# Performance work log

Hardware: AMD Instinct MI355X
Metric: run time of the kernel (lower is better)

The kernel has to match this reference:

```python
import jax, jax.numpy as jnp
import numpy as np

N = 50000       # nodes
E = 1600000     # edges (avg degree 32)
DIN = 64
DOUT = 64
DE = 16
ATT_SLOPE = 0.2   # leaky_relu slope inside attention (GAT standard)
ACT_SLOPE = 0.01  # F.leaky_relu default between layers


def setup_inputs() -> dict:
    key = jax.random.key(0)
    ks = jax.random.split(key, 16)

    def lin(k, i, o):
        return jax.random.normal(k, (i, o), jnp.float32) / np.sqrt(i).astype(np.float32)

    def vec(k, d):
        return jax.random.normal(k, (d,), jnp.float32) / np.sqrt(d).astype(np.float32)

    return {
        "X": jax.random.normal(ks[0], (N, DIN), jnp.float32),
        "edge_index": jax.random.randint(ks[1], (2, E), 0, N),
        "edge_attr": jax.random.normal(ks[2], (E, DE), jnp.float32),
        # layer 1 params
        "W1": lin(ks[3], DIN, DOUT), "We1": lin(ks[4], DE, DOUT),
        "as1": vec(ks[5], DOUT), "ad1": vec(ks[6], DOUT), "ae1": vec(ks[7], DOUT),
        "b1": jnp.zeros((DOUT,), jnp.float32),
        # layer 2 params
        "W2": lin(ks[8], DOUT, DOUT), "We2": lin(ks[9], DE, DOUT),
        "as2": vec(ks[10], DOUT), "ad2": vec(ks[11], DOUT), "ae2": vec(ks[12], DOUT),
        "b2": jnp.zeros((DOUT,), jnp.float32),
    }


def _gat_conv(x, src, dst, edge_attr, W, We, a_s, a_d, a_e, b):
    """GATConv with edge features, softmax attention over dst neighborhoods, max aggregation."""
    n = x.shape[0]
    h = x @ W                      # [N, DOUT]
    e = edge_attr @ We             # [E, DOUT]
    # per-edge attention logits
    logits = jax.nn.leaky_relu((h @ a_s)[src] + (h @ a_d)[dst] + e @ a_e, ATT_SLOPE)  # [E]
    # numerically-stable segment softmax over destination node
    m = jax.ops.segment_max(logits, dst, num_segments=n)      # [N]
    p = jnp.exp(logits - m[dst])                               # [E]
    s = jax.ops.segment_sum(p, dst, num_segments=n)            # [N]
    att = p / jnp.maximum(s[dst], 1e-16)                       # [E]
    msg = (h[src] + e) * att[:, None]                          # [E, DOUT]
    out = jax.ops.segment_max(msg, dst, num_segments=n)        # [N, DOUT], -inf for empty
    out = jnp.where(jnp.isfinite(out), out, 0.0)
    return out + b


def reference(X, edge_index, edge_attr,
              W1, We1, as1, ad1, ae1, b1,
              W2, We2, as2, ad2, ae2, b2):
    src, dst = edge_index[0], edge_index[1]
    c1 = _gat_conv(X, src, dst, edge_attr, W1, We1, as1, ad1, ae1, b1)
    c1 = jax.nn.leaky_relu(c1, ACT_SLOPE)
    c2 = _gat_conv(c1, src, dst, edge_attr, W2, We2, as2, ad2, ae2, b2)
    c2 = jax.nn.leaky_relu(c2, ACT_SLOPE)
    return c2
```

## Files before the change

kernel.cpp:

```cpp
#include <hip/hip_runtime.h>
#include <cstdint>
#include <cstddef>

#define NN 50000
#define EE 1600000
#define D  64
#define DE 16

typedef __attribute__((ext_vector_type(2))) float vf2;

__device__ __forceinline__ float bf2f(unsigned short u) {
    return __uint_as_float(((unsigned)u) << 16);
}
__device__ __forceinline__ unsigned short f2bf(float f) {
    unsigned u = __float_as_uint(f);
    unsigned r = u + 0x7FFFu + ((u >> 16) & 1u);
    return (unsigned short)(r >> 16);
}

#define HI_ILP 4
__global__ __launch_bounds__(256) void k_hist(const int* __restrict__ dst,
                                              int* __restrict__ counts) {
    int base = blockIdx.x * (256 * HI_ILP) + threadIdx.x;
    int dd[HI_ILP]; bool v[HI_ILP];
    #pragma unroll
    for (int j = 0; j < HI_ILP; j++) {
        int e = base + j * 256;
        v[j] = (e < EE);
        dd[j] = dst[v[j] ? e : 0];
    }
    #pragma unroll
    for (int j = 0; j < HI_ILP; j++)
        if (v[j]) atomicAdd(&counts[dd[j]], 1);
}

__global__ __launch_bounds__(256) void k_scanA(const int* counts, int* bsum) {
    __shared__ int tmp[256];
    int t = threadIdx.x, i = blockIdx.x * 256 + t;
    tmp[t] = (i < NN) ? counts[i] : 0;
    __syncthreads();
    for (int off = 128; off; off >>= 1) {
        if (t < off) tmp[t] += tmp[t + off];
        __syncthreads();
    }
    if (t == 0) bsum[blockIdx.x] = tmp[0];
}

__global__ __launch_bounds__(256) void k_scanB(int* bsum, int nchunks) {
    __shared__ int tmp[256];
    int t = threadIdx.x;
    int v = (t < nchunks) ? bsum[t] : 0;
    tmp[t] = v; __syncthreads();
    for (int off = 1; off < 256; off <<= 1) {
        int x = (t >= off) ? tmp[t - off] : 0;
        __syncthreads();
        tmp[t] += x;
        __syncthreads();
    }
    if (t < nchunks) bsum[t] = tmp[t] - v;
}

__global__ __launch_bounds__(256) void k_scanC(const int* counts, const int* bsumex,
                                               int* offsets, int* cursor) {
    __shared__ int tmp[256];
    int t = threadIdx.x, i = blockIdx.x * 256 + t;
    int v = (i < NN) ? counts[i] : 0;
    tmp[t] = v; __syncthreads();
    for (int off = 1; off < 256; off <<= 1) {
        int x = (t >= off) ? tmp[t - off] : 0;
        __syncthreads();
        tmp[t] += x;
        __syncthreads();
    }
    int excl = tmp[t] - v + bsumex[blockIdx.x];
    if (i < NN) { offsets[i] = excl; cursor[i] = excl; }
}

#define SC_ILP 8
__global__ __launch_bounds__(256) void k_scatter(const int* __restrict__ src,
                                                 const int* __restrict__ dst,
                                                 const float* __restrict__ ea,
                                                 const float* __restrict__ We1,
                                                 const float* __restrict__ ae1,
                                                 const float* __restrict__ We2,
                                                 const float* __restrict__ ae2,
                                                 int* __restrict__ cursor,
                                                 int4* __restrict__ recs) {
    __shared__ float wsh[32];
    int t = threadIdx.x;
    if (t < 32) {
        const float* We = (t < 16) ? We1 : We2;
        const float* ae = (t < 16) ? ae1 : ae2;
        int k = t & 15;
        float acc = 0.f;
        #pragma unroll
        for (int c = 0; c < 64; c++) acc += We[k * 64 + c] * ae[c];
        wsh[t] = acc;
    }
    __syncthreads();
    float w1r[16], w2r[16];
    #pragma unroll
    for (int j = 0; j < 16; j++) { w1r[j] = wsh[j]; w2r[j] = wsh[16 + j]; }

    int base = blockIdx.x * (256 * SC_ILP) + t;
    int dd[SC_ILP], ss[SC_ILP], pos[SC_ILP];
    bool v[SC_ILP];
    #pragma unroll
    for (int j = 0; j < SC_ILP; j++) {
        int e = base + j * 256;
        v[j] = (e < EE);
        int ec = v[j] ? e : 0;
        dd[j] = dst[ec];
        ss[j] = src[ec];
    }
    #pragma unroll
    for (int j = 0; j < SC_ILP; j++)
        if (v[j]) pos[j] = atomicAdd(&cursor[dd[j]], 1);
    #pragma unroll
    for (int j = 0; j < SC_ILP; j++) {
        if (!v[j]) continue;
        int e = base + j * 256;
        const float4* rp = (const float4*)(ea + (size_t)e * DE);
        float4 q0 = rp[0], q1 = rp[1], q2 = rp[2], q3 = rp[3];
        float ev[16] = {q0.x, q0.y, q0.z, q0.w, q1.x, q1.y, q1.z, q1.w,
                        q2.x, q2.y, q2.z, q2.w, q3.x, q3.y, q3.z, q3.w};
        float e1 = 0.f, e2 = 0.f;
        #pragma unroll
        for (int k2 = 0; k2 < 16; k2++) {
            e1 += ev[k2] * w1r[k2];
            e2 += ev[k2] * w2r[k2];
        }
        recs[pos[j]] = make_int4(ss[j], e, __float_as_int(e1), __float_as_int(e2));
    }
}

template<int IN_BF16>
__global__ __launch_bounds__(256, 4) void k_gemm(const void* xin, const float* W,
                                                 const float* a_s, const float* a_d,
                                                 unsigned short* h, float* hs, float* hd) {
    int t = threadIdx.x, lane = t & 63;
    int wid0 = blockIdx.x * 4 + (t >> 6);
    float Wcol[64];
    #pragma unroll
    for (int k = 0; k < 64; k++) Wcol[k] = W[k * 64 + lane];
    float asl = a_s[lane], adl = a_d[lane];
    for (int n0 = wid0; n0 < NN; n0 += 4096) {
        int n = __builtin_amdgcn_readfirstlane(n0);
        float acc = 0.f;
        if (IN_BF16) {
            const uint4* xr = (const uint4*)((const unsigned short*)xin + (size_t)n * 64);
            #pragma unroll
            for (int q = 0; q < 8; q++) {
                uint4 u = xr[q];
                unsigned uu[4] = {u.x, u.y, u.z, u.w};
                #pragma unroll
                for (int j = 0; j < 4; j++) {
                    acc += bf2f((unsigned short)(uu[j] & 0xFFFFu)) * Wcol[q * 8 + 2 * j];
                    acc += bf2f((unsigned short)(uu[j] >> 16))     * Wcol[q * 8 + 2 * j + 1];
                }
            }
        } else {
            const float4* xr = (const float4*)((const float*)xin + (size_t)n * 64);
            #pragma unroll
            for (int q = 0; q < 16; q++) {
                float4 u = xr[q];
                acc += u.x * Wcol[4 * q]     + u.y * Wcol[4 * q + 1]
                     + u.z * Wcol[4 * q + 2] + u.w * Wcol[4 * q + 3];
            }
        }
        h[(size_t)n * 64 + lane] = f2bf(acc);
        float ps = acc * asl, pd = acc * adl;
        #pragma unroll
        for (int off = 32; off; off >>= 1) {
            ps += __shfl_xor(ps, off);
            pd += __shfl_xor(pd, off);
        }
        if (lane == 0) { hs[n] = ps; hd[n] = pd; }
    }
}

template<int L2>
__global__ __launch_bounds__(256, 3) void k_gat(const int4* __restrict__ recs,
                                                const int* __restrict__ offsets,
                                                const int* __restrict__ counts,
                                                const float* __restrict__ hs,
                                                const float* __restrict__ hd,
                                                const unsigned short* __restrict__ h,
                                                const float* __restrict__ ea,
                                                const float* __restrict__ We,
                                                const float* __restrict__ b,
                                                void* __restrict__ outv) {
    __shared__ float4 eal[4][4][64];
    __shared__ float2 arx[4][64];
    int t = threadIdx.x, lane = t & 63, wv = t >> 6;
    int g = lane >> 4, cl = lane & 15;

    vf2 Wp[32];
    #pragma unroll
    for (int kp = 0; kp < 8; kp++) {
        float4 wa = *(const float4*)(We + (2 * kp) * 64 + 4 * cl);
        float4 wb = *(const float4*)(We + (2 * kp + 1) * 64 + 4 * cl);
        Wp[kp].x      = wa.x; Wp[kp].y      = wb.x;
        Wp[8 + kp].x  = wa.y; Wp[8 + kp].y  = wb.y;
        Wp[16 + kp].x = wa.z; Wp[16 + kp].y = wb.z;
        Wp[24 + kp].x = wa.w; Wp[24 + kp].y = wb.w;
    }

    int d = blockIdx.x * 4 + wv;
    int start = offsets[d];
    int deg = counts[d];

    if (deg == 0) {
        if (g == 0) {
            float4 bl = *(const float4*)(b + 4 * cl);
            float o0 = (bl.x >= 0.f) ? bl.x : 0.01f * bl.x;
            float o1 = (bl.y >= 0.f) ? bl.y : 0.01f * bl.y;
            float o2 = (bl.z >= 0.f) ? bl.z : 0.01f * bl.z;
            float o3 = (bl.w >= 0.f) ? bl.w : 0.01f * bl.w;
            size_t oidx = (size_t)d * D + 4 * cl;
            if (L2) *(float4*)((float*)outv + oidx) = make_float4(o0, o1, o2, o3);
            else {
                ushort4 ov = {f2bf(o0), f2bf(o1), f2bf(o2), f2bf(o3)};
                *(ushort4*)((unsigned short*)outv + oidx) = ov;
            }
        }
        return;
    }

    float hdv = hd[d];
    bool fast = (deg <= 64);
    float m, invs;

    float ninf = -__builtin_inff();
    float a0 = ninf, a1 = ninf, a2 = ninf, a3 = ninf;

    if (fast) {
        float lg = ninf;
        if (lane < deg) {
            int4 r = recs[start + lane];
            const float4* ep = (const float4*)(ea + (size_t)r.y * DE);
            float4 q0 = ep[0], q1 = ep[1], q2 = ep[2], q3 = ep[3];
            float hsv = hs[r.x];
            eal[wv][0][lane] = q0; eal[wv][1][lane] = q1;
            eal[wv][2][lane] = q2; eal[wv][3][lane] = q3;
            arx[wv][lane].y = __int_as_float(r.x);
            float ee = __int_as_float(L2 ? r.w : r.z);
            lg = hsv + hdv + ee;
            lg = (lg >= 0.f) ? lg : 0.2f * lg;
        }

        bool vC = (g < deg);
        int jC = vC ? g : 0;
        bool vN = (4 + g < deg);
        int jN = vN ? 4 + g : 0;
        int rxC = __float_as_int(arx[wv][jC].y);
        int rxN = __float_as_int(arx[wv][jN].y);
        ushort4 hvC = *(const ushort4*)(h + (size_t)rxC * D + 4 * cl);
        ushort4 hvN = *(const ushort4*)(h + (size_t)rxN * D + 4 * cl);

        m = lg;
        #pragma unroll
        for (int off = 32; off; off >>= 1) m = fmaxf(m, __shfl_xor(m, off));
        float p = __expf(lg - m);
        float s = p;
        #pragma unroll
        for (int off = 32; off; off >>= 1) s += __shfl_xor(s, off);
        invs = 1.0f / fmaxf(s, 1e-16f);
        if (lane < deg) arx[wv][lane].x = p * invs;

        float attC = arx[wv][jC].x;
        float attN = arx[wv][jN].x;

        for (int i = 0; i < deg; i += 4) {
            int jnn = i + 8 + g;
            bool vNN = (jnn < deg);
            int jNN = vNN ? jnn : 0;
            float2 arNN = arx[wv][jNN];
            int rxNN = __float_as_int(arNN.y);
            ushort4 hvNN = *(const ushort4*)(h + (size_t)rxNN * D + 4 * cl);

            vf2 acA = {0.f, 0.f}, acB = {0.f, 0.f}, acC2 = {0.f, 0.f}, acD = {0.f, 0.f};
            #pragma unroll
            for (int kq = 0; kq < 4; kq++) {
                float4 q = eal[wv][kq][jC];
                vf2 eA; eA.x = q.x; eA.y = q.y;
                vf2 eB; eB.x = q.z; eB.y = q.w;
                acA += eA * Wp[2 * kq];       acA += eB * Wp[2 * kq + 1];
                acB += eA * Wp[8 + 2 * kq];   acB += eB * Wp[8 + 2 * kq + 1];
                acC2 += eA * Wp[16 + 2 * kq]; acC2 += eB * Wp[16 + 2 * kq + 1];
                acD += eA * Wp[24 + 2 * kq];  acD += eB * Wp[24 + 2 * kq + 1];
            }
            float e0 = acA.x + acA.y, e1 = acB.x + acB.y;
            float e2 = acC2.x + acC2.y, e3 = acD.x + acD.y;
            float o0 = (bf2f(hvC.x) + e0) * attC;
            float o1 = (bf2f(hvC.y) + e1) * attC;
            float o2 = (bf2f(hvC.z) + e2) * attC;
            float o3 = (bf2f(hvC.w) + e3) * attC;
            if (vC) {
                a0 = fmaxf(a0, o0); a1 = fmaxf(a1, o1);
                a2 = fmaxf(a2, o2); a3 = fmaxf(a3, o3);
            }
            jC = jN; vC = vN; hvC = hvN; attC = attN;
            jN = jNN; vN = vNN; hvN = hvNN; attN = arNN.x;
        }
    } else {
        float mm = ninf, s = 0.f;
        for (int i = lane; i < deg; i += 64) {
            int4 r = recs[start + i];
            float ee = __int_as_float(L2 ? r.w : r.z);
            float lg = hs[r.x] + hdv + ee;
            lg = (lg >= 0.f) ? lg : 0.2f * lg;
            float mn = fmaxf(mm, lg);
            s = ((mm == mn) ? s : s * __expf(mm - mn)) + __expf(lg - mn);
            mm = mn;
        }
        #pragma unroll
        for (int off = 32; off; off >>= 1) {
            float m2 = __shfl_xor(mm, off);
            float s2 = __shfl_xor(s, off);
            float mn = fmaxf(mm, m2);
            float sa = (mm == mn) ? s : s * __expf(mm - mn);
            float sb = (m2 == mn) ? s2 : s2 * __expf(m2 - mn);
            s = sa + sb;
            mm = mn;
        }
        m = mm;
        invs = 1.0f / fmaxf(s, 1e-16f);

        for (int i = 0; i < deg; i += 4) {
            int j = i + g;
            bool valid = (j < deg);
            int jc = valid ? j : 0;
            int4 r = recs[start + jc];
            float ee = __int_as_float(L2 ? r.w : r.z);
            float lg = hs[r.x] + hdv + ee;
            lg = (lg >= 0.f) ? lg : 0.2f * lg;
            float att = __expf(lg - m) * invs;
            const float4* ep = (const float4*)(ea + (size_t)r.y * DE);
            float4 q0 = ep[0], q1 = ep[1], q2 = ep[2], q3 = ep[3];
            ushort4 hv = *(const ushort4*)(h + (size_t)r.x * D + 4 * cl);
            float4 qs[4] = {q0, q1, q2, q3};
            vf2 acA = {0.f, 0.f}, acB = {0.f, 0.f}, acC2 = {0.f, 0.f}, acD = {0.f, 0.f};
            #pragma unroll
            for (int kq = 0; kq < 4; kq++) {
                float4 q = qs[kq];
                vf2 eA; eA.x = q.x; eA.y = q.y;
                vf2 eB; eB.x = q.z; eB.y = q.w;
                acA += eA * Wp[2 * kq];       acA += eB * Wp[2 * kq + 1];
                acB += eA * Wp[8 + 2 * kq];   acB += eB * Wp[8 + 2 * kq + 1];
                acC2 += eA * Wp[16 + 2 * kq]; acC2 += eB * Wp[16 + 2 * kq + 1];
                acD += eA * Wp[24 + 2 * kq];  acD += eB * Wp[24 + 2 * kq + 1];
            }
            float e0 = acA.x + acA.y, e1 = acB.x + acB.y;
            float e2 = acC2.x + acC2.y, e3 = acD.x + acD.y;
            float o0 = (bf2f(hv.x) + e0) * att;
            float o1 = (bf2f(hv.y) + e1) * att;
            float o2 = (bf2f(hv.z) + e2) * att;
            float o3 = (bf2f(hv.w) + e3) * att;
            if (valid) {
                a0 = fmaxf(a0, o0); a1 = fmaxf(a1, o1);
                a2 = fmaxf(a2, o2); a3 = fmaxf(a3, o3);
            }
        }
    }

    #pragma unroll
    for (int off = 16; off <= 32; off <<= 1) {
        a0 = fmaxf(a0, __shfl_xor(a0, off));
        a1 = fmaxf(a1, __shfl_xor(a1, off));
        a2 = fmaxf(a2, __shfl_xor(a2, off));
        a3 = fmaxf(a3, __shfl_xor(a3, off));
    }

    if (g == 0) {
        float4 bl = *(const float4*)(b + 4 * cl);
        float o0 = a0 + bl.x, o1 = a1 + bl.y;
        float o2 = a2 + bl.z, o3 = a3 + bl.w;
        o0 = (o0 >= 0.f) ? o0 : 0.01f * o0;
        o1 = (o1 >= 0.f) ? o1 : 0.01f * o1;
        o2 = (o2 >= 0.f) ? o2 : 0.01f * o2;
        o3 = (o3 >= 0.f) ? o3 : 0.01f * o3;
        size_t oidx = (size_t)d * D + 4 * cl;
        if (L2) {
            *(float4*)((float*)outv + oidx) = make_float4(o0, o1, o2, o3);
        } else {
            ushort4 ov = {f2bf(o0), f2bf(o1), f2bf(o2), f2bf(o3)};
            *(ushort4*)((unsigned short*)outv + oidx) = ov;
        }
    }
}

extern "C" void kernel_launch(void* const* d_in, const int* in_sizes, int n_in,
                              void* d_out, int out_size, void* d_ws, size_t ws_size,
                              hipStream_t stream) {
    const float* X   = (const float*)d_in[0];
    const int*   eix = (const int*)d_in[1];
    const float* ea  = (const float*)d_in[2];
    const float* W1  = (const float*)d_in[3];
    const float* We1 = (const float*)d_in[4];
    const float* as1 = (const float*)d_in[5];
    const float* ad1 = (const float*)d_in[6];
    const float* ae1 = (const float*)d_in[7];
    const float* b1  = (const float*)d_in[8];
    const float* W2  = (const float*)d_in[9];
    const float* We2 = (const float*)d_in[10];
    const float* as2 = (const float*)d_in[11];
    const float* ad2 = (const float*)d_in[12];
    const float* ae2 = (const float*)d_in[13];
    const float* b2  = (const float*)d_in[14];

    const int* src = eix;
    const int* dst = eix + EE;

    char* w = (char*)d_ws;
    int4* recs = (int4*)w;               w += (size_t)EE * 16;
    unsigned short* hA = (unsigned short*)w; w += (size_t)NN * D * 2;
    unsigned short* hB = (unsigned short*)w; w += (size_t)NN * D * 2;
    float* hs = (float*)w;               w += (size_t)NN * 4;
    float* hd = (float*)w;               w += (size_t)NN * 4;
    int* counts = (int*)w;               w += (size_t)NN * 4;
    int* offsets = (int*)w;              w += (size_t)NN * 4;
    int* cursor = (int*)w;               w += (size_t)NN * 4;
    int* bsum = (int*)w;                 w += 256 * 4;

    const int nchunks = (NN + 255) / 256;
    const int nhblk = (EE + 256 * HI_ILP - 1) / (256 * HI_ILP);
    const int nsblk = (EE + 256 * SC_ILP - 1) / (256 * SC_ILP);

    hipMemsetAsync(counts, 0, (size_t)NN * 4, stream);
    k_hist<<<nhblk, 256, 0, stream>>>(dst, counts);
    k_scanA<<<nchunks, 256, 0, stream>>>(counts, bsum);
    k_scanB<<<1, 256, 0, stream>>>(bsum, nchunks);
    k_scanC<<<nchunks, 256, 0, stream>>>(counts, bsum, offsets, cursor);
    k_scatter<<<nsblk, 256, 0, stream>>>(src, dst, ea, We1, ae1, We2, ae2, cursor, recs);

    k_gemm<0><<<1024, 256, 0, stream>>>(X, W1, as1, ad1, hA, hs, hd);
    k_gat<0><<<NN / 4, 256, 0, stream>>>(recs, offsets, counts, hs, hd, hA, ea, We1, b1, hB);
    k_gemm<1><<<1024, 256, 0, stream>>>(hB, W2, as2, ad2, hB, hs, hd);
    k_gat<1><<<NN / 4, 256, 0, stream>>>(recs, offsets, counts, hs, hd, hB, ea, We2, b2,
                                         (float*)d_out);
}
```

Baseline: 627.2 us.

## Fold block-sum scan into scanC and merge layer-1 GEMM with edge scatter

Removes the separate single-block scan kernel by having every scanC block redundantly scan the block sums in shared memory. Merges the layer-1 node GEMM and the edge scatter into one launch: the first 1024 blocks compute h, hs and hd, and the remaining blocks do the CSR scatter. The two independent phases can then overlap on the GPU and two launches go away. Scatter ILP drops from 8 to 2, which raises the scatter block count, and shared memory per block grows to 16KB for all blocks, including the scatter ones that do not need it.

```diff
diff --git a/kernel.cpp b/kernel.cpp
--- a/kernel.cpp
+++ b/kernel.cpp
@@ -46,24 +46,22 @@
     if (t == 0) bsum[blockIdx.x] = tmp[0];
 }
 
-__global__ __launch_bounds__(256) void k_scanB(int* bsum, int nchunks) {
+__global__ __launch_bounds__(256) void k_scanC(const int* counts, const int* bsum,
+                                               int nchunks, int* offsets, int* cursor) {
+    __shared__ int tmpb[256];
     __shared__ int tmp[256];
     int t = threadIdx.x;
-    int v = (t < nchunks) ? bsum[t] : 0;
-    tmp[t] = v; __syncthreads();
+    int bv = (t < nchunks) ? bsum[t] : 0;
+    tmpb[t] = bv; __syncthreads();
     for (int off = 1; off < 256; off <<= 1) {
-        int x = (t >= off) ? tmp[t - off] : 0;
-        __syncthreads();
-        tmp[t] += x;
-        __syncthreads();
-    }
-    if (t < nchunks) bsum[t] = tmp[t] - v;
-}
-
-__global__ __launch_bounds__(256) void k_scanC(const int* counts, const int* bsumex,
-                                               int* offsets, int* cursor) {
-    __shared__ int tmp[256];
-    int t = threadIdx.x, i = blockIdx.x * 256 + t;
+        int x = (t >= off) ? tmpb[t - off] : 0;
+        __syncthreads();
+        tmpb[t] += x;
+        __syncthreads();
+    }
+    int base = (blockIdx.x > 0) ? tmpb[blockIdx.x - 1] : 0;
+
+    int i = blockIdx.x * 256 + t;
     int v = (i < NN) ? counts[i] : 0;
     tmp[t] = v; __syncthreads();
     for (int off = 1; off < 256; off <<= 1) {
@@ -72,22 +70,55 @@
         tmp[t] += x;
         __syncthreads();
     }
-    int excl = tmp[t] - v + bsumex[blockIdx.x];
+    int excl = tmp[t] - v + base;
     if (i < NN) { offsets[i] = excl; cursor[i] = excl; }
 }
 
-#define SC_ILP 8
-__global__ __launch_bounds__(256) void k_scatter(const int* __restrict__ src,
-                                                 const int* __restrict__ dst,
-                                                 const float* __restrict__ ea,
-                                                 const float* __restrict__ We1,
-                                                 const float* __restrict__ ae1,
-                                                 const float* __restrict__ We2,
-                                                 const float* __restrict__ ae2,
-                                                 int* __restrict__ cursor,
-                                                 int4* __restrict__ recs) {
-    __shared__ float wsh[32];
+#define SC_ILP 2
+__global__ __launch_bounds__(256) void k_scatter_gemm(
+        const int* __restrict__ src, const int* __restrict__ dst,
+        const float* __restrict__ ea,
+        const float* __restrict__ We1, const float* __restrict__ ae1,
+        const float* __restrict__ We2, const float* __restrict__ ae2,
+        int* __restrict__ cursor, int4* __restrict__ recs,
+        const float* __restrict__ X, const float* __restrict__ W,
+        const float* __restrict__ a_s, const float* __restrict__ a_d,
+        unsigned short* __restrict__ h, float* __restrict__ hs,
+        float* __restrict__ hd) {
+    __shared__ float sh[64 * 64];
     int t = threadIdx.x;
+
+    if (blockIdx.x < 1024) {
+        for (int i = t; i < 1024; i += 256)
+            ((float4*)sh)[i] = ((const float4*)W)[i];
+        __syncthreads();
+        int lane = t & 63;
+        int wid0 = blockIdx.x * 4 + (t >> 6);
+        float asl = a_s[lane], adl = a_d[lane];
+        for (int n0 = wid0; n0 < NN; n0 += 4096) {
+            int n = __builtin_amdgcn_readfirstlane(n0);
+            const float4* xr = (const float4*)(X + (size_t)n * 64);
+            float acc = 0.f;
+            #pragma unroll
+            for (int q = 0; q < 16; q++) {
+                float4 u = xr[q];
+                acc += u.x * sh[(4 * q) * 64 + lane]
+                     + u.y * sh[(4 * q + 1) * 64 + lane]
+                     + u.z * sh[(4 * q + 2) * 64 + lane]
+                     + u.w * sh[(4 * q + 3) * 64 + lane];
+            }
+            h[(size_t)n * 64 + lane] = f2bf(acc);
+            float ps = acc * asl, pd = acc * adl;
+            #pragma unroll
+            for (int off = 32; off; off >>= 1) {
+                ps += __shfl_xor(ps, off);
+                pd += __shfl_xor(pd, off);
+            }
+            if (lane == 0) { hs[n] = ps; hd[n] = pd; }
+        }
+        return;
+    }
+
     if (t < 32) {
         const float* We = (t < 16) ? We1 : We2;
         const float* ae = (t < 16) ? ae1 : ae2;
@@ -95,14 +126,14 @@
         float acc = 0.f;
         #pragma unroll
         for (int c = 0; c < 64; c++) acc += We[k * 64 + c] * ae[c];
-        wsh[t] = acc;
+        sh[t] = acc;
     }
     __syncthreads();
     float w1r[16], w2r[16];
     #pragma unroll
-    for (int j = 0; j < 16; j++) { w1r[j] = wsh[j]; w2r[j] = wsh[16 + j]; }
-
-    int base = blockIdx.x * (256 * SC_ILP) + t;
+    for (int j = 0; j < 16; j++) { w1r[j] = sh[j]; w2r[j] = sh[16 + j]; }
+
+    int base = (blockIdx.x - 1024) * (256 * SC_ILP) + t;
     int dd[SC_ILP], ss[SC_ILP], pos[SC_ILP];
     bool v[SC_ILP];
     #pragma unroll
@@ -430,11 +461,12 @@
     hipMemsetAsync(counts, 0, (size_t)NN * 4, stream);
     k_hist<<<nhblk, 256, 0, stream>>>(dst, counts);
     k_scanA<<<nchunks, 256, 0, stream>>>(counts, bsum);
-    k_scanB<<<1, 256, 0, stream>>>(bsum, nchunks);
-    k_scanC<<<nchunks, 256, 0, stream>>>(counts, bsum, offsets, cursor);
-    k_scatter<<<nsblk, 256, 0, stream>>>(src, dst, ea, We1, ae1, We2, ae2, cursor, recs);
-
-    k_gemm<0><<<1024, 256, 0, stream>>>(X, W1, as1, ad1, hA, hs, hd);
+    k_scanC<<<nchunks, 256, 0, stream>>>(counts, bsum, nchunks, offsets, cursor);
+
+    k_scatter_gemm<<<1024 + nsblk, 256, 0, stream>>>(src, dst, ea,
+                                                     We1, ae1, We2, ae2,
+                                                     cursor, recs,
+                                                     X, W1, as1, ad1, hA, hs, hd);
     k_gat<0><<<NN / 4, 256, 0, stream>>>(recs, offsets, counts, hs, hd, hA, ea, We1, b1, hB);
     k_gemm<1><<<1024, 256, 0, stream>>>(hB, W2, as2, ad2, hB, hs, hd);
     k_gat<1><<<NN / 4, 256, 0, stream>>>(recs, offsets, counts, hs, hd, hB, ea, We2, b2,
```

Result: faster. 565.5 us (-9.8%).
